# Kernel tuning notes

Hardware: AMD Instinct MI355X
Metric: run time of the kernel (lower is better)

The kernel has to match this reference:

```python
import jax, jax.numpy as jnp
import numpy as np

IN_FEATURES = 4096
OUT_FEATURES = 11008
GROUP_SIZE = 64
NUM_GROUPS = (OUT_FEATURES * IN_FEATURES) // GROUP_SIZE  # 704512, no padding


def setup_inputs() -> dict:
    key = jax.random.key(0)
    k_x, k_q, k_s, k_m, k_b = jax.random.split(key, 5)
    x = jax.random.normal(k_x, (2, 2048, IN_FEATURES), dtype=jnp.float32)
    weight_q3 = jax.random.randint(k_q, (NUM_GROUPS, GROUP_SIZE), 0, 8, dtype=jnp.int32)
    # positive scales, matching clamp(min=1e-8) in the quantizer
    weight_scales = jax.random.uniform(k_s, (NUM_GROUPS,), dtype=jnp.float32, minval=0.01, maxval=1.0)
    weight_sparse_mask = jax.random.uniform(k_m, (NUM_GROUPS, GROUP_SIZE)) < 0.1
    bias = jax.random.normal(k_b, (OUT_FEATURES,), dtype=jnp.float32)
    return {"x": x, "weight_q3": weight_q3, "weight_scales": weight_scales,
            "weight_sparse_mask": weight_sparse_mask, "bias": bias}


def _dequant(weight_q3, weight_scales, weight_sparse_mask):
    # x_norm = q/7; deq = x_norm*2*s - s = (2*q/7 - 1) * s ; masked -> 0
    scales = weight_scales[:, None]  # [G, 1]
    deq = (weight_q3.astype(jnp.float32) * (2.0 / 7.0) - 1.0) * scales
    deq = jnp.where(weight_sparse_mask, 0.0, deq)
    return deq.reshape(OUT_FEATURES, IN_FEATURES)


def reference(x, weight_q3, weight_scales, weight_sparse_mask, bias):
    W = _dequant(weight_q3, weight_scales, weight_sparse_mask)  # [O, I] fp32
    # F.linear: y = x @ W^T + b
    return jnp.einsum('bsi,oi->bso', x, W) + bias
```

## Files before the change

### kernel.cpp

```cpp
#include <hip/hip_runtime.h>
#include <hip/hip_bf16.h>

#define IN_F   4096
#define OUT_F  11008
#define MROWS  4096
#define BM     256
#define BN     256
#define BK     64
#define NT     (IN_F / BK)
#define CVT_BLOCKS ((MROWS * IN_F) / (256 * 8))
#define DEQ_BLOCKS ((OUT_F * IN_F) / (256 * 8))

typedef __bf16 bf16x8 __attribute__((ext_vector_type(8)));
typedef float  f32x4  __attribute__((ext_vector_type(4)));

__global__ __launch_bounds__(256) void k_prep(const float* __restrict__ x,
                                              const int* __restrict__ q,
                                              const int* __restrict__ mask,
                                              const float* __restrict__ scales,
                                              __hip_bfloat16* __restrict__ xb,
                                              __hip_bfloat16* __restrict__ Wb)
{
    if (blockIdx.x < CVT_BLOCKS) {
        const long long t    = (long long)blockIdx.x * 256 + threadIdx.x;
        const long long base = t * 8;
        const float4 a = *(const float4*)(x + base);
        const float4 b = *(const float4*)(x + base + 4);
        float f[8] = {a.x, a.y, a.z, a.w, b.x, b.y, b.z, b.w};
        union { int4 v; __hip_bfloat16 h[8]; } u;
#pragma unroll
        for (int j = 0; j < 8; ++j) u.h[j] = __float2bfloat16(f[j]);
        *(int4*)(xb + base) = u.v;
    } else {
        const long long t    = (long long)(blockIdx.x - CVT_BLOCKS) * 256 + threadIdx.x;
        const long long base = t * 8;
        const int   g = (int)(base >> 6);
        const float s = scales[g];
        const int4 q0 = *(const int4*)(q + base);
        const int4 q1 = *(const int4*)(q + base + 4);
        const int4 m0 = *(const int4*)(mask + base);
        const int4 m1 = *(const int4*)(mask + base + 4);
        const float c = 2.0f / 7.0f;
        int qa[8] = {q0.x, q0.y, q0.z, q0.w, q1.x, q1.y, q1.z, q1.w};
        int ma[8] = {m0.x, m0.y, m0.z, m0.w, m1.x, m1.y, m1.z, m1.w};
        union { int4 v; __hip_bfloat16 h[8]; } u;
#pragma unroll
        for (int j = 0; j < 8; ++j) {
            float w = ma[j] ? 0.0f : ((float)qa[j] * c - 1.0f) * s;
            u.h[j] = __float2bfloat16(w);
        }
        *(int4*)(Wb + base) = u.v;
    }
}

__device__ __forceinline__ void gl_lds16(const __hip_bfloat16* g, __hip_bfloat16* l)
{
    __builtin_amdgcn_global_load_lds(
        (const __attribute__((address_space(1))) void*)g,
        (__attribute__((address_space(3))) void*)l,
        16, 0, 0);
}

#define LDA(S, I, K) bA[S][K] = *(const bf16x8*)(Asb + ((I) * 32 + wm16 + lr) * 64 + ((((quad) + (K) * 4) ^ swr) * 8))
#define LDB(J, K)    bB[J][K] = *(const bf16x8*)(Bsb + ((J) * 64 + wn16 + lr) * 64 + ((((quad) + (K) * 4) ^ swr) * 8))

#define MMQ(IB, JB) do { \
    _Pragma("unroll") \
    for (int _jj = 0; _jj < 2; ++_jj) \
        _Pragma("unroll") \
        for (int _ii = 0; _ii < 4; ++_ii) \
            _Pragma("unroll") \
            for (int _kk = 0; _kk < 2; ++_kk) \
                acc[(IB) + _ii][(JB) + _jj] = __builtin_amdgcn_mfma_f32_16x16x32_bf16( \
                    bB[(JB) + _jj][_kk], bA[_ii][_kk], acc[(IB) + _ii][(JB) + _jj], 0, 0, 0); \
} while (0)

#define STAGE(gbase, ldsbase, k0, HF) do { \
    _Pragma("unroll") \
    for (int _t = 0; _t < 2; ++_t) { \
        const int _c = wave * 2 + _t; \
        const int _r = (HF) * 128 + _c * 8 + lrow; \
        gl_lds16((gbase) + (size_t)_r * IN_F + (k0) + lcol, (ldsbase) + _c * 512); \
    } \
} while (0)

#define TILE(BUF, T, SP1, SP2, VMODE) do { \
    const __hip_bfloat16* Asb = &As[(BUF)][0]; \
    const __hip_bfloat16* Bsb = &Bs[(BUF)][0]; \
     \
    LDA(0,0,0); LDA(0,0,1); LDA(1,1,0); LDA(1,1,1); \
    LDA(2,2,0); LDA(2,2,1); LDA(3,3,0); LDA(3,3,1); \
    LDB(0,0);   LDB(0,1);   LDB(1,0);   LDB(1,1); \
    if (SP1) STAGE(Bblk, &Bs[(BUF)^1][0], ((T)+1)*BK, 0); \
    __builtin_amdgcn_s_barrier(); \
    asm volatile("s_waitcnt lgkmcnt(0)" ::: "memory"); \
    __builtin_amdgcn_s_setprio(1); MMQ(0,0); __builtin_amdgcn_s_setprio(0); \
    __builtin_amdgcn_s_barrier(); \
     \
    LDB(2,0); LDB(2,1); LDB(3,0); LDB(3,1); \
    if (SP2) STAGE(Ablk, &As[(BUF)][0], ((T)+2)*BK, 0); \
    __builtin_amdgcn_s_barrier(); \
    asm volatile("s_waitcnt lgkmcnt(0)" ::: "memory"); \
    __builtin_amdgcn_s_setprio(1); MMQ(0,2); __builtin_amdgcn_s_setprio(0); \
    __builtin_amdgcn_s_barrier(); \
     \
    LDA(0,4,0); LDA(0,4,1); LDA(1,5,0); LDA(1,5,1); \
    LDA(2,6,0); LDA(2,6,1); LDA(3,7,0); LDA(3,7,1); \
    if (SP2) STAGE(Bblk, &Bs[(BUF)][128*64], ((T)+2)*BK, 1); \
    __builtin_amdgcn_s_barrier(); \
    asm volatile("s_waitcnt lgkmcnt(0)" ::: "memory"); \
    __builtin_amdgcn_s_setprio(1); MMQ(4,0); __builtin_amdgcn_s_setprio(0); \
    __builtin_amdgcn_s_barrier(); \
     \
    if (SP2) STAGE(Ablk, &As[(BUF)][128*64], ((T)+2)*BK, 1); \
    __builtin_amdgcn_s_barrier(); \
    if ((VMODE) == 2)      asm volatile("s_waitcnt vmcnt(6)" ::: "memory"); \
    else if ((VMODE) == 1) asm volatile("s_waitcnt vmcnt(0)" ::: "memory"); \
    __builtin_amdgcn_s_setprio(1); MMQ(4,2); __builtin_amdgcn_s_setprio(0); \
    __builtin_amdgcn_s_barrier(); \
} while (0)

__global__ __launch_bounds__(512, 2) void k_gemm(const __hip_bfloat16* __restrict__ A,
                                                 const __hip_bfloat16* __restrict__ B,
                                                 const float* __restrict__ bias,
                                                 float* __restrict__ C)
{
    __shared__ __align__(16) __hip_bfloat16 As[2][BM * BK];
    __shared__ __align__(16) __hip_bfloat16 Bs[2][BN * BK];

    const int tid  = threadIdx.x;
    const int lane = tid & 63;
    const int wave = tid >> 6;
    const int wm16 = (wave >> 2) * 16;
    const int wn16 = (wave & 3) * 16;
    const int quad = lane >> 4;
    const int lr   = lane & 15;
    const int swr  = lr & 7;
    const int lrow = lane >> 3;
    const int lcol = ((lane & 7) ^ lrow) * 8;

    const int orig = blockIdx.x;
    const int swz  = (orig & 7) * (688 >> 3) + (orig >> 3);
    const int bm   = swz & 15;
    const int bn   = swz >> 4;

    const __hip_bfloat16* Ablk = A + (size_t)bm * BM * IN_F;
    const __hip_bfloat16* Bblk = B + (size_t)bn * BN * IN_F;

    bf16x8 bA[4][2];
    bf16x8 bB[4][2];
    f32x4  acc[8][4];
#pragma unroll
    for (int i = 0; i < 8; ++i)
#pragma unroll
        for (int j = 0; j < 4; ++j)
            acc[i][j] = (f32x4){0.f, 0.f, 0.f, 0.f};

    STAGE(Bblk, &Bs[0][0],      0,  0);
    STAGE(Ablk, &As[0][0],      0,  0);
    STAGE(Bblk, &Bs[0][128*64], 0,  1);
    STAGE(Ablk, &As[0][128*64], 0,  1);
    STAGE(Ablk, &As[1][0],      BK, 0);
    STAGE(Bblk, &Bs[1][128*64], BK, 1);
    STAGE(Ablk, &As[1][128*64], BK, 1);
    asm volatile("s_waitcnt vmcnt(6)" ::: "memory");
    __builtin_amdgcn_s_barrier();

    for (int u = 0; u < (NT - 2) / 2; ++u) {
        const int t0 = 2 * u;
        TILE(0, t0,     1, 1, 2);
        TILE(1, t0 + 1, 1, 1, 2);
    }
    TILE(0, NT - 2, 1, 0, 1);
    TILE(1, NT - 1, 0, 0, 0);

#pragma unroll
    for (int j = 0; j < 4; ++j) {
        const int o = bn * BN + j * 64 + wn16 + quad * 4;
        const float4 bv = *(const float4*)(bias + o);
#pragma unroll
        for (int i = 0; i < 8; ++i) {
            const int s = bm * BM + i * 32 + wm16 + lr;
            float4 v;
            v.x = acc[i][j][0] + bv.x;
            v.y = acc[i][j][1] + bv.y;
            v.z = acc[i][j][2] + bv.z;
            v.w = acc[i][j][3] + bv.w;
            *(float4*)(C + (size_t)s * OUT_F + o) = v;
        }
    }
}

extern "C" void kernel_launch(void* const* d_in, const int* in_sizes, int n_in,
                              void* d_out, int out_size, void* d_ws, size_t ws_size,
                              hipStream_t stream)
{
    const float* x      = (const float*)d_in[0];
    const int*   q      = (const int*)d_in[1];
    const float* scales = (const float*)d_in[2];
    const int*   mask   = (const int*)d_in[3];
    const float* bias   = (const float*)d_in[4];
    float* out          = (float*)d_out;

    __hip_bfloat16* xb = (__hip_bfloat16*)d_ws;
    __hip_bfloat16* Wb = xb + (size_t)MROWS * IN_F;

    k_prep<<<CVT_BLOCKS + DEQ_BLOCKS, 256, 0, stream>>>(x, q, mask, scales, xb, Wb);

    k_gemm<<<dim3(688), dim3(512), 0, stream>>>(xb, Wb, bias, out);
}
```

Measured before the change: 878.4 us.

## Prefetch next tile's B fragments early and use grid-stride prep kernel

```diff
diff --git a/kernel.cpp b/kernel.cpp
--- a/kernel.cpp
+++ b/kernel.cpp
@@ -8,8 +8,9 @@
 #define BN     256
 #define BK     64
 #define NT     (IN_F / BK)
-#define CVT_BLOCKS ((MROWS * IN_F) / (256 * 8))
-#define DEQ_BLOCKS ((OUT_F * IN_F) / (256 * 8))
+#define CVT_CHUNKS (((long long)MROWS * IN_F) / 8)
+#define TOT_CHUNKS (((long long)(MROWS + OUT_F) * IN_F) / 8)
+#define PREP_GRID  2048
 
 typedef __bf16 bf16x8 __attribute__((ext_vector_type(8)));
 typedef float  f32x4  __attribute__((ext_vector_type(4)));
@@ -21,35 +22,36 @@
                                               __hip_bfloat16* __restrict__ xb,
                                               __hip_bfloat16* __restrict__ Wb)
 {
-    if (blockIdx.x < CVT_BLOCKS) {
-        const long long t    = (long long)blockIdx.x * 256 + threadIdx.x;
-        const long long base = t * 8;
-        const float4 a = *(const float4*)(x + base);
-        const float4 b = *(const float4*)(x + base + 4);
-        float f[8] = {a.x, a.y, a.z, a.w, b.x, b.y, b.z, b.w};
-        union { int4 v; __hip_bfloat16 h[8]; } u;
-#pragma unroll
-        for (int j = 0; j < 8; ++j) u.h[j] = __float2bfloat16(f[j]);
-        *(int4*)(xb + base) = u.v;
-    } else {
-        const long long t    = (long long)(blockIdx.x - CVT_BLOCKS) * 256 + threadIdx.x;
-        const long long base = t * 8;
-        const int   g = (int)(base >> 6);
-        const float s = scales[g];
-        const int4 q0 = *(const int4*)(q + base);
-        const int4 q1 = *(const int4*)(q + base + 4);
-        const int4 m0 = *(const int4*)(mask + base);
-        const int4 m1 = *(const int4*)(mask + base + 4);
-        const float c = 2.0f / 7.0f;
-        int qa[8] = {q0.x, q0.y, q0.z, q0.w, q1.x, q1.y, q1.z, q1.w};
-        int ma[8] = {m0.x, m0.y, m0.z, m0.w, m1.x, m1.y, m1.z, m1.w};
-        union { int4 v; __hip_bfloat16 h[8]; } u;
-#pragma unroll
-        for (int j = 0; j < 8; ++j) {
-            float w = ma[j] ? 0.0f : ((float)qa[j] * c - 1.0f) * s;
-            u.h[j] = __float2bfloat16(w);
+    const long long stride = (long long)PREP_GRID * 256;
+    for (long long c = (long long)blockIdx.x * 256 + threadIdx.x; c < TOT_CHUNKS; c += stride) {
+        if (c < CVT_CHUNKS) {
+            const long long base = c * 8;
+            const float4 a = *(const float4*)(x + base);
+            const float4 b = *(const float4*)(x + base + 4);
+            float f[8] = {a.x, a.y, a.z, a.w, b.x, b.y, b.z, b.w};
+            union { int4 v; __hip_bfloat16 h[8]; } u;
+#pragma unroll
+            for (int j = 0; j < 8; ++j) u.h[j] = __float2bfloat16(f[j]);
+            *(int4*)(xb + base) = u.v;
+        } else {
+            const long long base = (c - CVT_CHUNKS) * 8;
+            const int   g = (int)(base >> 6);
+            const float s = scales[g];
+            const int4 q0 = *(const int4*)(q + base);
+            const int4 q1 = *(const int4*)(q + base + 4);
+            const int4 m0 = *(const int4*)(mask + base);
+            const int4 m1 = *(const int4*)(mask + base + 4);
+            const float cc = 2.0f / 7.0f;
+            int qa[8] = {q0.x, q0.y, q0.z, q0.w, q1.x, q1.y, q1.z, q1.w};
+            int ma[8] = {m0.x, m0.y, m0.z, m0.w, m1.x, m1.y, m1.z, m1.w};
+            union { int4 v; __hip_bfloat16 h[8]; } u;
+#pragma unroll
+            for (int j = 0; j < 8; ++j) {
+                float w = ma[j] ? 0.0f : ((float)qa[j] * cc - 1.0f) * s;
+                u.h[j] = __float2bfloat16(w);
+            }
+            *(int4*)(Wb + base) = u.v;
         }
-        *(int4*)(Wb + base) = u.v;
     }
 }
 
@@ -60,9 +62,6 @@
         (__attribute__((address_space(3))) void*)l,
         16, 0, 0);
 }
-
-#define LDA(S, I, K) bA[S][K] = *(const bf16x8*)(Asb + ((I) * 32 + wm16 + lr) * 64 + ((((quad) + (K) * 4) ^ swr) * 8))
-#define LDB(J, K)    bB[J][K] = *(const bf16x8*)(Bsb + ((J) * 64 + wn16 + lr) * 64 + ((((quad) + (K) * 4) ^ swr) * 8))
 
 #define MMQ(IB, JB) do { \
     _Pragma("unroll") \
@@ -84,28 +83,33 @@
     } \
 } while (0)
 
-#define TILE(BUF, T, SP1, SP2, VMODE) do { \
-    const __hip_bfloat16* Asb = &As[(BUF)][0]; \
-    const __hip_bfloat16* Bsb = &Bs[(BUF)][0]; \
-     \
-    LDA(0,0,0); LDA(0,0,1); LDA(1,1,0); LDA(1,1,1); \
-    LDA(2,2,0); LDA(2,2,1); LDA(3,3,0); LDA(3,3,1); \
-    LDB(0,0);   LDB(0,1);   LDB(1,0);   LDB(1,1); \
+#define TILE(BUF, T, SP1, SP2, VMODE, RD4) do { \
+    const __hip_bfloat16* pA  = &As[(BUF)][0] + offA;         \
+    const __hip_bfloat16* pB  = &Bs[(BUF)][0] + offB; \
+    const __hip_bfloat16* pBn = &Bs[(BUF)^1][0] + offB; \
+     \
+    bA[0][0] = *(const bf16x8*)(pA + x0);        bA[0][1] = *(const bf16x8*)(pA + x1); \
+    bA[1][0] = *(const bf16x8*)(pA + x0 + 2048); bA[1][1] = *(const bf16x8*)(pA + x1 + 2048); \
+    bA[2][0] = *(const bf16x8*)(pA + x0 + 4096); bA[2][1] = *(const bf16x8*)(pA + x1 + 4096); \
+    bA[3][0] = *(const bf16x8*)(pA + x0 + 6144); bA[3][1] = *(const bf16x8*)(pA + x1 + 6144); \
     if (SP1) STAGE(Bblk, &Bs[(BUF)^1][0], ((T)+1)*BK, 0); \
     __builtin_amdgcn_s_barrier(); \
     asm volatile("s_waitcnt lgkmcnt(0)" ::: "memory"); \
     __builtin_amdgcn_s_setprio(1); MMQ(0,0); __builtin_amdgcn_s_setprio(0); \
     __builtin_amdgcn_s_barrier(); \
      \
-    LDB(2,0); LDB(2,1); LDB(3,0); LDB(3,1); \
+    bB[2][0] = *(const bf16x8*)(pB + x0 + 8192);  bB[2][1] = *(const bf16x8*)(pB + x1 + 8192); \
+    bB[3][0] = *(const bf16x8*)(pB + x0 + 12288); bB[3][1] = *(const bf16x8*)(pB + x1 + 12288); \
     if (SP2) STAGE(Ablk, &As[(BUF)][0], ((T)+2)*BK, 0); \
     __builtin_amdgcn_s_barrier(); \
     asm volatile("s_waitcnt lgkmcnt(0)" ::: "memory"); \
     __builtin_amdgcn_s_setprio(1); MMQ(0,2); __builtin_amdgcn_s_setprio(0); \
     __builtin_amdgcn_s_barrier(); \
      \
-    LDA(0,4,0); LDA(0,4,1); LDA(1,5,0); LDA(1,5,1); \
-    LDA(2,6,0); LDA(2,6,1); LDA(3,7,0); LDA(3,7,1); \
+    bA[0][0] = *(const bf16x8*)(pA + x0 + 8192);  bA[0][1] = *(const bf16x8*)(pA + x1 + 8192); \
+    bA[1][0] = *(const bf16x8*)(pA + x0 + 10240); bA[1][1] = *(const bf16x8*)(pA + x1 + 10240); \
+    bA[2][0] = *(const bf16x8*)(pA + x0 + 12288); bA[2][1] = *(const bf16x8*)(pA + x1 + 12288); \
+    bA[3][0] = *(const bf16x8*)(pA + x0 + 14336); bA[3][1] = *(const bf16x8*)(pA + x1 + 14336); \
     if (SP2) STAGE(Bblk, &Bs[(BUF)][128*64], ((T)+2)*BK, 1); \
     __builtin_amdgcn_s_barrier(); \
     asm volatile("s_waitcnt lgkmcnt(0)" ::: "memory"); \
@@ -116,6 +120,11 @@
     __builtin_amdgcn_s_barrier(); \
     if ((VMODE) == 2)      asm volatile("s_waitcnt vmcnt(6)" ::: "memory"); \
     else if ((VMODE) == 1) asm volatile("s_waitcnt vmcnt(0)" ::: "memory"); \
+    if (RD4) { \
+        bB[0][0] = *(const bf16x8*)(pBn + x0);        bB[0][1] = *(const bf16x8*)(pBn + x1); \
+        bB[1][0] = *(const bf16x8*)(pBn + x0 + 4096); bB[1][1] = *(const bf16x8*)(pBn + x1 + 4096); \
+        __builtin_amdgcn_sched_barrier(0);   \
+    } \
     __builtin_amdgcn_s_setprio(1); MMQ(4,2); __builtin_amdgcn_s_setprio(0); \
     __builtin_amdgcn_s_barrier(); \
 } while (0)
@@ -139,6 +148,11 @@
     const int lrow = lane >> 3;
     const int lcol = ((lane & 7) ^ lrow) * 8;
 
+    const int offA = (wm16 + lr) * 64;
+    const int offB = (wn16 + lr) * 64;
+    const int x0   = (quad ^ swr) * 8;
+    const int x1   = x0 ^ 32;
+
     const int orig = blockIdx.x;
     const int swz  = (orig & 7) * (688 >> 3) + (orig >> 3);
     const int bm   = swz & 15;
@@ -165,14 +179,19 @@
     STAGE(Ablk, &As[1][128*64], BK, 1);
     asm volatile("s_waitcnt vmcnt(6)" ::: "memory");
     __builtin_amdgcn_s_barrier();
+    {
+        const __hip_bfloat16* pB0 = &Bs[0][0] + offB;
+        bB[0][0] = *(const bf16x8*)(pB0 + x0);        bB[0][1] = *(const bf16x8*)(pB0 + x1);
+        bB[1][0] = *(const bf16x8*)(pB0 + x0 + 4096); bB[1][1] = *(const bf16x8*)(pB0 + x1 + 4096);
+    }
 
     for (int u = 0; u < (NT - 2) / 2; ++u) {
         const int t0 = 2 * u;
-        TILE(0, t0,     1, 1, 2);
-        TILE(1, t0 + 1, 1, 1, 2);
-    }
-    TILE(0, NT - 2, 1, 0, 1);
-    TILE(1, NT - 1, 0, 0, 0);
+        TILE(0, t0,     1, 1, 2, 1);
+        TILE(1, t0 + 1, 1, 1, 2, 1);
+    }
+    TILE(0, NT - 2, 1, 0, 1, 1);
+    TILE(1, NT - 1, 0, 0, 0, 0);
 
 #pragma unroll
     for (int j = 0; j < 4; ++j) {
@@ -205,7 +224,7 @@
     __hip_bfloat16* xb = (__hip_bfloat16*)d_ws;
     __hip_bfloat16* Wb = xb + (size_t)MROWS * IN_F;
 
-    k_prep<<<CVT_BLOCKS + DEQ_BLOCKS, 256, 0, stream>>>(x, q, mask, scales, xb, Wb);
+    k_prep<<<PREP_GRID, 256, 0, stream>>>(x, q, mask, scales, xb, Wb);
 
     k_gemm<<<dim3(688), dim3(512), 0, stream>>>(xb, Wb, bias, out);
 }
```

Result: faster. 834.2 us (-5.0%).
